# Optimization experiments

Measured on AMD Instinct MI355X. Metric: run time of the kernel, lower is better.

## Reference

```python
import jax, jax.numpy as jnp
import numpy as np
from jax import lax

ALPHA = 1.5
N_ITER = 100


def entmax(z, alpha=ALPHA, n_iter=N_ITER):
    # z: [B, Sq, Sk] scores. Bisection for the entmax threshold tau.
    z = (alpha - 1.0) * z.astype(jnp.float32)
    S = z.shape[-1]
    z_max = jnp.max(z, axis=-1, keepdims=True)          # [B, Sq, 1]
    tau_min = z_max - 1.0
    tau_max = z_max - np.float32(S ** (1.0 - alpha))
    inv = 1.0 / (alpha - 1.0)                            # = 2.0 for alpha=1.5

    def body(carry, _):
        tmin, tmax, _ = carry
        tau = (tmin + tmax) * 0.5
        p = jnp.maximum(z - tau, 0.0) ** inv             # [B, Sq, Sk]
        Z = jnp.sum(p, axis=-1, keepdims=True)           # [B, Sq, 1]
        tmin = jnp.where(Z >= 1.0, tau, tmin)
        tmax = jnp.where(Z < 1.0, tau, tmax)
        return (tmin, tmax, tau), None

    init = (tau_min, tau_max, (tau_min + tau_max) * 0.5)
    (tmin, tmax, tau), _ = lax.scan(jax.checkpoint(body), init, None, length=n_iter)
    # faithful to the TF code: final output uses p, Z from the LAST iteration's tau
    p = jnp.maximum(z - tau, 0.0) ** inv
    Z = jnp.sum(p, axis=-1, keepdims=True)
    return p / Z


def setup_inputs() -> dict:
    key = jax.random.key(0)
    kq, kk, kv = jax.random.split(key, 3)
    B, S, D = 8, 2048, 128
    return {
        "query": jax.random.normal(kq, (B, S, D), dtype=jnp.float32),
        "key": jax.random.normal(kk, (B, S, D), dtype=jnp.float32),
        "value": jax.random.normal(kv, (B, S, D), dtype=jnp.float32),
    }


def reference(query, key, value):
    scores = jnp.einsum("bqd,bkd->bqk", query, key)      # QK^T, no scaling (as in source)
    weights = entmax(scores, alpha=ALPHA, n_iter=N_ITER)
    return jnp.einsum("bqk,bkd->bqd", weights, value)
```

## Files before the change

kernel.cpp:

```cpp
#include <hip/hip_runtime.h>

#define BB 8
#define SS 2048
#define DD 128
#define ROWS 16
#define NW 8
#define CTW 16

typedef short bf16x8 __attribute__((ext_vector_type(8)));
typedef float f32x4 __attribute__((ext_vector_type(4)));

template <int I> struct IC { static constexpr int value = I; };
template <int I, int N, typename F>
__device__ __forceinline__ void sfor(F&& f) {
  if constexpr (I < N) { f(IC<I>{}); sfor<I + 1, N>((F&&)f); }
}

__device__ __forceinline__ short f2bf(float x) {
  return __builtin_bit_cast(short, (__bf16)x);
}

__device__ __forceinline__ void stage_tile(const short* g, short* l) {
#pragma unroll
  for (int s = 0; s < 4; ++s) {
    __builtin_amdgcn_global_load_lds(
        (const __attribute__((address_space(1))) void*)(g + (s << 9)),
        (__attribute__((address_space(3))) void*)(l + (s << 9)), 16, 0, 0);
  }
}

__global__ __launch_bounds__(256)
void ksplit(const float* __restrict__ K, short* __restrict__ Khi) {
  const int lin = blockIdx.x * 256 + threadIdx.x;
  const int r   = lin >> 4;
  const int c8  = lin & 15;
  const float4 v0 = *(const float4*)(K + (size_t)lin * 8);
  const float4 v1 = *(const float4*)(K + (size_t)lin * 8 + 4);
  bf16x8 h;
  h[0] = f2bf(v0.x); h[1] = f2bf(v0.y); h[2] = f2bf(v0.z); h[3] = f2bf(v0.w);
  h[4] = f2bf(v1.x); h[5] = f2bf(v1.y); h[6] = f2bf(v1.z); h[7] = f2bf(v1.w);
  const int bct  = r >> 4;
  const int m16  = r & 15;
  const int s    = c8 >> 2;
  const int quad = c8 & 3;
  const size_t out = ((((size_t)bct * 4 + s) * 64) + quad * 16 + m16) * 8;
  *(bf16x8*)(Khi + out) = h;
}

__global__ __launch_bounds__(512) __attribute__((amdgpu_waves_per_eu(3, 4)))
void attn(const float* __restrict__ Q, const short* __restrict__ Khi,
          const float* __restrict__ K, const float* __restrict__ V,
          float* __restrict__ Out) {
  __shared__ short kring[NW][2][2048];
  __shared__ unsigned short Qs[ROWS][136];
  __shared__ float rbuf[ROWS][64];
  __shared__ int   scol[ROWS][64];
  __shared__ float exM[NW][ROWS];
  __shared__ int   rcnt[ROWS];
  __shared__ int   rovf[ROWS];
  __shared__ float tauB[ROWS], ZB[ROWS];

  const int tid  = threadIdx.x;
  const int lane = tid & 63;
  const int wid  = __builtin_amdgcn_readfirstlane(tid >> 6);
  const int quad = lane >> 4, m16 = lane & 15;
  const int b    = blockIdx.x & 7;
  const int qt   = blockIdx.x >> 3;

  const float* Qb = Q + (size_t)(b * SS + qt * ROWS) * DD;
  const float* Kb = K + (size_t)b * SS * DD;
  const float* Vb = V + (size_t)b * SS * DD;
  float*       Ob = Out + (size_t)(b * SS + qt * ROWS) * DD;
  const short* KHb = Khi + (size_t)b * SS * DD;

  if (tid < ROWS) { rcnt[tid] = 0; rovf[tid] = 0; }

  {
    const int row = tid >> 5, d = (tid & 31) * 4;
    const float4 v = *(const float4*)&Qb[row * DD + d];
    ushort4 h;
    h.x = (unsigned short)f2bf(0.5f * v.x);
    h.y = (unsigned short)f2bf(0.5f * v.y);
    h.z = (unsigned short)f2bf(0.5f * v.z);
    h.w = (unsigned short)f2bf(0.5f * v.w);
    *(ushort4*)&Qs[row][d] = h;
  }
  __syncthreads();

  bf16x8 qh[4];
#pragma unroll
  for (int s = 0; s < 4; ++s)
    qh[s] = *(const bf16x8*)&Qs[m16][s * 32 + quad * 8];

  short* ring0 = &kring[wid][0][0];
  short* ring1 = &kring[wid][1][0];
  const short* gw = KHb + ((size_t)(wid * CTW) << 11) + lane * 8;

  stage_tile(gw + 0 * 2048, ring0);
  stage_tile(gw + 1 * 2048, ring1);

  f32x4 acc[CTW];
  sfor<0, CTW>([&](auto ic) {
    constexpr int i = ic.value;
    if constexpr (i < CTW - 1) asm volatile("s_waitcnt vmcnt(4)" ::: "memory");
    else                       asm volatile("s_waitcnt vmcnt(0)" ::: "memory");
    const short* sbl = ((i & 1) ? ring1 : ring0) + lane * 8;
    f32x4 c = {0.f, 0.f, 0.f, 0.f};
    sfor<0, 4>([&](auto sc) {
      constexpr int s = sc.value;
      const bf16x8 bh = *(const bf16x8*)(sbl + (s << 9));
      c = __builtin_amdgcn_mfma_f32_16x16x32_bf16(qh[s], bh, c, 0, 0, 0);
    });
    acc[i] = c;
    if constexpr (i + 2 < CTW) {
      asm volatile("s_waitcnt lgkmcnt(0)" ::: "memory");
      stage_tile(gw + (i + 2) * 2048, (i & 1) ? ring1 : ring0);
    }
  });

  float mx[4] = {-1e38f, -1e38f, -1e38f, -1e38f};
  sfor<0, CTW>([&](auto ic) {
#pragma unroll
    for (int j = 0; j < 4; ++j) mx[j] = fmaxf(mx[j], acc[ic.value][j]);
  });
#pragma unroll
  for (int j = 0; j < 4; ++j)
#pragma unroll
    for (int s = 1; s <= 8; s <<= 1) mx[j] = fmaxf(mx[j], __shfl_xor(mx[j], s));
  if (m16 == 0) {
#pragma unroll
    for (int j = 0; j < 4; ++j) exM[wid][4 * quad + j] = mx[j];
  }
  __syncthreads();
  float M4[4];
#pragma unroll
  for (int j = 0; j < 4; ++j) {
    float m = -1e38f;
#pragma unroll
    for (int w = 0; w < NW; ++w) m = fmaxf(m, exM[w][4 * quad + j]);
    M4[j] = m;
  }

  sfor<0, CTW>([&](auto ic) {
    constexpr int i = ic.value;
    const int col = wid * 256 + i * 16 + m16;
#pragma unroll
    for (int j = 0; j < 4; ++j) {
      const int row = 4 * quad + j;
      if (acc[i][j] > M4[j] - 1.25f) {
        const int pos = atomicAdd(&rcnt[row], 1);
        if (pos < 64) { scol[row][pos] = col; rbuf[row][pos] = acc[i][j]; }
        else rovf[row] = 1;
      }
    }
  });
  __syncthreads();

  const int rr32 = lane >> 5;
  const int row  = 2 * wid + rr32;
  const int l32  = lane & 31;
  const int nA = rcnt[2 * wid]     < 64 ? rcnt[2 * wid]     : 64;
  const int nB = rcnt[2 * wid + 1] < 64 ? rcnt[2 * wid + 1] : 64;
  const int nr  = rr32 ? nB : nA;
  const int nmx = nA > nB ? nA : nB;

  {
    const float4 q4 = *(const float4*)&Qb[row * DD + l32 * 4];
    for (int i = 0; i < nmx; ++i) {
      const bool act = i < nr;
      const int c = act ? scol[row][i] : scol[row][0];
      const float4 k4 = *(const float4*)&Kb[(size_t)c * DD + l32 * 4];
      float t = q4.x * k4.x + q4.y * k4.y + q4.z * k4.z + q4.w * k4.w;
#pragma unroll
      for (int s = 1; s <= 16; s <<= 1) t += __shfl_xor(t, s);
      if (act && l32 == 0) rbuf[row][i] = 0.5f * t;
    }
  }

  {
    const float z0 = (l32 < nr)      ? rbuf[row][l32]      : -1e38f;
    const float z1 = (l32 + 32 < nr) ? rbuf[row][l32 + 32] : -1e38f;
    float k0 = 0.f, S10 = 0.f, S20 = 0.f, nb0 = -1e38f;
    float k1 = 0.f, S11 = 0.f, S21 = 0.f, nb1 = -1e38f;
    for (int j = 0; j < nr; ++j) {
      const float w = rbuf[row][j];
      const bool ge0 = (w > z0) || (w == z0 && j <= l32);
      k0  += ge0 ? 1.f : 0.f;
      S10 += ge0 ? w : 0.f;
      S20  = ge0 ? fmaf(w, w, S20) : S20;
      nb0  = (!ge0 && w > nb0) ? w : nb0;
      const bool ge1 = (w > z1) || (w == z1 && j <= l32 + 32);
      k1  += ge1 ? 1.f : 0.f;
      S11 += ge1 ? w : 0.f;
      S21  = ge1 ? fmaf(w, w, S21) : S21;
      nb1  = (!ge1 && w > nb1) ? w : nb1;
    }
    const float d0 = fmaxf(fmaf(S10, S10, -k0 * (S20 - 1.f)), 0.f);
    const float d1 = fmaxf(fmaf(S11, S11, -k1 * (S21 - 1.f)), 0.f);
    const float tau0 = (S10 - __builtin_sqrtf(d0)) / fmaxf(k0, 1.f);
    const float tau1 = (S11 - __builtin_sqrtf(d1)) / fmaxf(k1, 1.f);
    const bool v0b = z0 > tau0, v1b = z1 > tau1;
    const bool v0  = v0b && (nb0 <= tau0);
    const bool v1  = v1b && (nb1 <= tau1);
    float tv = fmaxf(v0 ? tau0 : -1e38f, v1 ? tau1 : -1e38f);
    float tb = fmaxf(v0b ? tau0 : -1e38f, v1b ? tau1 : -1e38f);
#pragma unroll
    for (int s = 1; s <= 16; s <<= 1) {
      tv = fmaxf(tv, __shfl_xor(tv, s));
      tb = fmaxf(tb, __shfl_xor(tb, s));
    }
    const float tau = (tv > -1e37f) ? tv : tb;
    const float p0 = fmaxf(z0 - tau, 0.f);
    const float p1 = fmaxf(z1 - tau, 0.f);
    float zp = fmaf(p0, p0, p1 * p1);
#pragma unroll
    for (int s = 1; s <= 16; s <<= 1) zp += __shfl_xor(zp, s);
    if (l32 == 0) { tauB[row] = tau; ZB[row] = zp; }
  }

  if (!rovf[row]) {
    const float tau = tauB[row];
    const float iz  = 1.0f / ZB[row];
    float4 o = {0.f, 0.f, 0.f, 0.f};
    for (int i = 0; i < nr; ++i) {
      const float rv = rbuf[row][i];
      const float tt = fmaxf(rv - tau, 0.f);
      const float pi = tt * tt * iz;
      const int   c  = scol[row][i];
      const float4 v4 = *(const float4*)&Vb[(size_t)c * DD + l32 * 4];
      o.x = fmaf(pi, v4.x, o.x);
      o.y = fmaf(pi, v4.y, o.y);
      o.z = fmaf(pi, v4.z, o.z);
      o.w = fmaf(pi, v4.w, o.w);
    }
    *(float4*)&Ob[row * DD + l32 * 4] = o;
  }

#pragma unroll
  for (int rr = 0; rr < 2; ++rr) {
    const int frow = 2 * wid + rr;
    if (!rovf[frow]) continue;
    float* zr = (float*)&kring[wid][0][0];
    for (int c0 = 0; c0 < 32; ++c0) {
      const int c = c0 * 64 + lane;
      const float* kp = &Kb[(size_t)c * DD];
      float t = 0.f;
      for (int d = 0; d < DD; d += 4) {
        const float4 qv = *(const float4*)&Qb[frow * DD + d];
        const float4 kv = *(const float4*)&kp[d];
        t = fmaf(qv.x, kv.x, t); t = fmaf(qv.y, kv.y, t);
        t = fmaf(qv.z, kv.z, t); t = fmaf(qv.w, kv.w, t);
      }
      zr[c] = 0.5f * t;
    }
    float Mr = -1e38f;
    for (int c0 = 0; c0 < 32; ++c0) Mr = fmaxf(Mr, zr[c0 * 64 + lane]);
#pragma unroll
    for (int s = 1; s <= 32; s <<= 1) Mr = fmaxf(Mr, __shfl_xor(Mr, s));
    float tmn = Mr - 1.0f, tmx = Mr - 0.022097086912079608f;
    float tau = 0.5f * (tmn + tmx), Zr = 0.f;
    for (int it = 0; it < 100; ++it) {
      tau = 0.5f * (tmn + tmx);
      float zp = 0.f;
      for (int c0 = 0; c0 < 32; ++c0) {
        const float tt = fmaxf(zr[c0 * 64 + lane] - tau, 0.f);
        zp = fmaf(tt, tt, zp);
      }
#pragma unroll
      for (int s = 1; s <= 32; s <<= 1) zp += __shfl_xor(zp, s);
      Zr = zp;
      const float nmn = (zp >= 1.f) ? tau : tmn;
      const float nmx2 = (zp >= 1.f) ? tmx : tau;
      const bool ch = (nmn != tmn) || (nmx2 != tmx);
      tmn = nmn; tmx = nmx2;
      if (!__any(ch)) break;
    }
    const float iz = 1.0f / Zr;
    float2 o = {0.f, 0.f};
    for (int c = 0; c < SS; ++c) {
      const float tt = fmaxf(zr[c] - tau, 0.f);
      if (tt > 0.f) {
        const float pi = tt * tt * iz;
        const float2 v2 = *(const float2*)&Vb[(size_t)c * DD + lane * 2];
        o.x = fmaf(pi, v2.x, o.x);
        o.y = fmaf(pi, v2.y, o.y);
      }
    }
    *(float2*)&Ob[frow * DD + lane * 2] = o;
  }
}

extern "C" void kernel_launch(void* const* d_in, const int* in_sizes, int n_in,
                              void* d_out, int out_size, void* d_ws, size_t ws_size,
                              hipStream_t stream) {
  const float* Q = (const float*)d_in[0];
  const float* K = (const float*)d_in[1];
  const float* V = (const float*)d_in[2];
  float* out = (float*)d_out;
  short* Khi = (short*)d_ws;

  hipLaunchKernelGGL(ksplit, dim3(BB * SS * DD / (256 * 8)), dim3(256), 0, stream,
                     K, Khi);
  hipLaunchKernelGGL(attn, dim3(BB * (SS / ROWS)), dim3(512), 0, stream,
                     Q, Khi, K, V, out);
}
```

Measured before the change: 117.0 us.

## Deepen K-tile ring to four stages and restructure candidate rescoring and PV loops

Grows the per-wave LDS ring for the bf16 K tiles from two to four buffers, so four tiles are in flight and the vmcnt waits are adjusted to match. The fp32 rescoring of candidate columns changes from one candidate per iteration with a 32-lane shuffle reduction to one candidate per lane with a full 128-element serial dot product. The PV accumulation loop is unrolled by four with masked tail entries so more V loads are in flight. The larger ring doubles the LDS footprint, which may lower occupancy, and the per-lane dot products read K rows with strided, uncoalesced access.

```diff
diff --git a/kernel.cpp b/kernel.cpp
--- a/kernel.cpp
+++ b/kernel.cpp
@@ -18,6 +18,13 @@
 
 __device__ __forceinline__ short f2bf(float x) {
   return __builtin_bit_cast(short, (__bf16)x);
+}
+
+template <int N> __device__ __forceinline__ void wait_vm() {
+  if constexpr (N >= 12)      asm volatile("s_waitcnt vmcnt(12)" ::: "memory");
+  else if constexpr (N == 8)  asm volatile("s_waitcnt vmcnt(8)" ::: "memory");
+  else if constexpr (N == 4)  asm volatile("s_waitcnt vmcnt(4)" ::: "memory");
+  else                        asm volatile("s_waitcnt vmcnt(0)" ::: "memory");
 }
 
 __device__ __forceinline__ void stage_tile(const short* g, short* l) {
@@ -51,7 +58,7 @@
 void attn(const float* __restrict__ Q, const short* __restrict__ Khi,
           const float* __restrict__ K, const float* __restrict__ V,
           float* __restrict__ Out) {
-  __shared__ short kring[NW][2][2048];
+  __shared__ short kring[NW][4][2048];
   __shared__ unsigned short Qs[ROWS][136];
   __shared__ float rbuf[ROWS][64];
   __shared__ int   scol[ROWS][64];
@@ -92,19 +99,19 @@
   for (int s = 0; s < 4; ++s)
     qh[s] = *(const bf16x8*)&Qs[m16][s * 32 + quad * 8];
 
-  short* ring0 = &kring[wid][0][0];
-  short* ring1 = &kring[wid][1][0];
+  short* ring = &kring[wid][0][0];
   const short* gw = KHb + ((size_t)(wid * CTW) << 11) + lane * 8;
 
-  stage_tile(gw + 0 * 2048, ring0);
-  stage_tile(gw + 1 * 2048, ring1);
+  sfor<0, 4>([&](auto pc) {
+    constexpr int p = pc.value;
+    stage_tile(gw + p * 2048, ring + p * 2048);
+  });
 
   f32x4 acc[CTW];
   sfor<0, CTW>([&](auto ic) {
     constexpr int i = ic.value;
-    if constexpr (i < CTW - 1) asm volatile("s_waitcnt vmcnt(4)" ::: "memory");
-    else                       asm volatile("s_waitcnt vmcnt(0)" ::: "memory");
-    const short* sbl = ((i & 1) ? ring1 : ring0) + lane * 8;
+    wait_vm<(15 - i >= 3 ? 12 : 4 * (15 - i))>();
+    const short* sbl = ring + ((i & 3) << 11) + lane * 8;
     f32x4 c = {0.f, 0.f, 0.f, 0.f};
     sfor<0, 4>([&](auto sc) {
       constexpr int s = sc.value;
@@ -112,9 +119,9 @@
       c = __builtin_amdgcn_mfma_f32_16x16x32_bf16(qh[s], bh, c, 0, 0, 0);
     });
     acc[i] = c;
-    if constexpr (i + 2 < CTW) {
+    if constexpr (i + 4 < CTW) {
       asm volatile("s_waitcnt lgkmcnt(0)" ::: "memory");
-      stage_tile(gw + (i + 2) * 2048, (i & 1) ? ring1 : ring0);
+      stage_tile(gw + (i + 4) * 2048, ring + ((i & 3) << 11));
     }
   });
 
@@ -162,18 +169,36 @@
   const int nA = rcnt[2 * wid]     < 64 ? rcnt[2 * wid]     : 64;
   const int nB = rcnt[2 * wid + 1] < 64 ? rcnt[2 * wid + 1] : 64;
   const int nr  = rr32 ? nB : nA;
-  const int nmx = nA > nB ? nA : nB;
 
   {
-    const float4 q4 = *(const float4*)&Qb[row * DD + l32 * 4];
-    for (int i = 0; i < nmx; ++i) {
-      const bool act = i < nr;
-      const int c = act ? scol[row][i] : scol[row][0];
-      const float4 k4 = *(const float4*)&Kb[(size_t)c * DD + l32 * 4];
-      float t = q4.x * k4.x + q4.y * k4.y + q4.z * k4.z + q4.w * k4.w;
-#pragma unroll
-      for (int s = 1; s <= 16; s <<= 1) t += __shfl_xor(t, s);
-      if (act && l32 == 0) rbuf[row][i] = 0.5f * t;
+    const float4* qp4 = (const float4*)&Qb[row * DD];
+    if (l32 < nr) {
+      const float4* kp4 = (const float4*)&Kb[(size_t)scol[row][l32] * DD];
+      f32x4 t = {0.f, 0.f, 0.f, 0.f};
+#pragma unroll 8
+      for (int d = 0; d < 32; ++d) {
+        const float4 qv = qp4[d];
+        const float4 kv = kp4[d];
+        t[0] = fmaf(qv.x, kv.x, t[0]);
+        t[1] = fmaf(qv.y, kv.y, t[1]);
+        t[2] = fmaf(qv.z, kv.z, t[2]);
+        t[3] = fmaf(qv.w, kv.w, t[3]);
+      }
+      rbuf[row][l32] = 0.5f * ((t[0] + t[1]) + (t[2] + t[3]));
+    }
+    if (nr > 32 && l32 + 32 < nr) {
+      const float4* kp4 = (const float4*)&Kb[(size_t)scol[row][l32 + 32] * DD];
+      f32x4 t = {0.f, 0.f, 0.f, 0.f};
+#pragma unroll 8
+      for (int d = 0; d < 32; ++d) {
+        const float4 qv = qp4[d];
+        const float4 kv = kp4[d];
+        t[0] = fmaf(qv.x, kv.x, t[0]);
+        t[1] = fmaf(qv.y, kv.y, t[1]);
+        t[2] = fmaf(qv.z, kv.z, t[2]);
+        t[3] = fmaf(qv.w, kv.w, t[3]);
+      }
+      rbuf[row][l32 + 32] = 0.5f * ((t[0] + t[1]) + (t[2] + t[3]));
     }
   }
 
@@ -222,16 +247,21 @@
     const float tau = tauB[row];
     const float iz  = 1.0f / ZB[row];
     float4 o = {0.f, 0.f, 0.f, 0.f};
-    for (int i = 0; i < nr; ++i) {
-      const float rv = rbuf[row][i];
-      const float tt = fmaxf(rv - tau, 0.f);
-      const float pi = tt * tt * iz;
-      const int   c  = scol[row][i];
-      const float4 v4 = *(const float4*)&Vb[(size_t)c * DD + l32 * 4];
-      o.x = fmaf(pi, v4.x, o.x);
-      o.y = fmaf(pi, v4.y, o.y);
-      o.z = fmaf(pi, v4.z, o.z);
-      o.w = fmaf(pi, v4.w, o.w);
+    for (int i = 0; i < nr; i += 4) {
+#pragma unroll
+      for (int k = 0; k < 4; ++k) {
+        const bool act = (i + k) < nr;
+        const int  idx = act ? i + k : 0;
+        const float rv = rbuf[row][idx];
+        const float tt = fmaxf(rv - tau, 0.f);
+        const float pi = act ? tt * tt * iz : 0.f;
+        const int   c  = scol[row][idx];
+        const float4 v4 = *(const float4*)&Vb[(size_t)c * DD + l32 * 4];
+        o.x = fmaf(pi, v4.x, o.x);
+        o.y = fmaf(pi, v4.y, o.y);
+        o.z = fmaf(pi, v4.z, o.z);
+        o.w = fmaf(pi, v4.w, o.w);
+      }
     }
     *(float4*)&Ob[row * DD + l32 * 4] = o;
   }
```

Result: slower. 136.8 us (+17.0%).

## Process 32 query rows per block, reusing each staged K tile across two MFMA groups

Applied to the files above, without the earlier changes.

Each block now handles 32 query rows instead of 16. Every staged bf16 K tile feeds two MFMA accumulators, which halves the number of blocks and the total K streaming traffic. To keep register pressure down, the score tiles are kept as packed bf16 pairs instead of f32, and the row max is computed while the MFMAs run. In exchange, the candidate-selection threshold is widened to allow for the bf16 rounding, the per-wave refinement and PV work doubles, and fewer blocks may leave CUs underused.

```diff
diff --git a/kernel.cpp b/kernel.cpp
--- a/kernel.cpp
+++ b/kernel.cpp
@@ -3,7 +3,7 @@
 #define BB 8
 #define SS 2048
 #define DD 128
-#define ROWS 16
+#define ROWS 32
 #define NW 8
 #define CTW 16
 
@@ -18,6 +18,10 @@
 
 __device__ __forceinline__ short f2bf(float x) {
   return __builtin_bit_cast(short, (__bf16)x);
+}
+__device__ __forceinline__ unsigned pk2(float a, float b) {
+  return (unsigned)(unsigned short)f2bf(a) |
+         ((unsigned)(unsigned short)f2bf(b) << 16);
 }
 
 __device__ __forceinline__ void stage_tile(const short* g, short* l) {
@@ -76,21 +80,29 @@
   if (tid < ROWS) { rcnt[tid] = 0; rovf[tid] = 0; }
 
   {
-    const int row = tid >> 5, d = (tid & 31) * 4;
-    const float4 v = *(const float4*)&Qb[row * DD + d];
-    ushort4 h;
-    h.x = (unsigned short)f2bf(0.5f * v.x);
-    h.y = (unsigned short)f2bf(0.5f * v.y);
-    h.z = (unsigned short)f2bf(0.5f * v.z);
-    h.w = (unsigned short)f2bf(0.5f * v.w);
-    *(ushort4*)&Qs[row][d] = h;
+    const int row = tid >> 4, d = (tid & 15) * 8;
+    const float4 v0 = *(const float4*)&Qb[row * DD + d];
+    const float4 v1 = *(const float4*)&Qb[row * DD + d + 4];
+    ushort4 h0, h1;
+    h0.x = (unsigned short)f2bf(0.5f * v0.x);
+    h0.y = (unsigned short)f2bf(0.5f * v0.y);
+    h0.z = (unsigned short)f2bf(0.5f * v0.z);
+    h0.w = (unsigned short)f2bf(0.5f * v0.w);
+    h1.x = (unsigned short)f2bf(0.5f * v1.x);
+    h1.y = (unsigned short)f2bf(0.5f * v1.y);
+    h1.z = (unsigned short)f2bf(0.5f * v1.z);
+    h1.w = (unsigned short)f2bf(0.5f * v1.w);
+    *(ushort4*)&Qs[row][d]     = h0;
+    *(ushort4*)&Qs[row][d + 4] = h1;
   }
   __syncthreads();
 
-  bf16x8 qh[4];
-#pragma unroll
-  for (int s = 0; s < 4; ++s)
-    qh[s] = *(const bf16x8*)&Qs[m16][s * 32 + quad * 8];
+  bf16x8 qh[2][4];
+#pragma unroll
+  for (int g = 0; g < 2; ++g)
+#pragma unroll
+    for (int s = 0; s < 4; ++s)
+      qh[g][s] = *(const bf16x8*)&Qs[g * 16 + m16][s * 32 + quad * 8];
 
   short* ring0 = &kring[wid][0][0];
   short* ring1 = &kring[wid][1][0];
@@ -99,146 +111,173 @@
   stage_tile(gw + 0 * 2048, ring0);
   stage_tile(gw + 1 * 2048, ring1);
 
-  f32x4 acc[CTW];
+  unsigned zpk[2][CTW][2];
+  float mx[2][4] = {{-1e38f, -1e38f, -1e38f, -1e38f},
+                    {-1e38f, -1e38f, -1e38f, -1e38f}};
+
   sfor<0, CTW>([&](auto ic) {
     constexpr int i = ic.value;
     if constexpr (i < CTW - 1) asm volatile("s_waitcnt vmcnt(4)" ::: "memory");
     else                       asm volatile("s_waitcnt vmcnt(0)" ::: "memory");
     const short* sbl = ((i & 1) ? ring1 : ring0) + lane * 8;
-    f32x4 c = {0.f, 0.f, 0.f, 0.f};
+    f32x4 cA = {0.f, 0.f, 0.f, 0.f};
+    f32x4 cB = {0.f, 0.f, 0.f, 0.f};
     sfor<0, 4>([&](auto sc) {
       constexpr int s = sc.value;
       const bf16x8 bh = *(const bf16x8*)(sbl + (s << 9));
-      c = __builtin_amdgcn_mfma_f32_16x16x32_bf16(qh[s], bh, c, 0, 0, 0);
+      cA = __builtin_amdgcn_mfma_f32_16x16x32_bf16(qh[0][s], bh, cA, 0, 0, 0);
+      cB = __builtin_amdgcn_mfma_f32_16x16x32_bf16(qh[1][s], bh, cB, 0, 0, 0);
     });
-    acc[i] = c;
+#pragma unroll
+    for (int j = 0; j < 4; ++j) {
+      mx[0][j] = fmaxf(mx[0][j], cA[j]);
+      mx[1][j] = fmaxf(mx[1][j], cB[j]);
+    }
+    zpk[0][i][0] = pk2(cA[0], cA[1]);
+    zpk[0][i][1] = pk2(cA[2], cA[3]);
+    zpk[1][i][0] = pk2(cB[0], cB[1]);
+    zpk[1][i][1] = pk2(cB[2], cB[3]);
     if constexpr (i + 2 < CTW) {
       asm volatile("s_waitcnt lgkmcnt(0)" ::: "memory");
       stage_tile(gw + (i + 2) * 2048, (i & 1) ? ring1 : ring0);
     }
   });
 
-  float mx[4] = {-1e38f, -1e38f, -1e38f, -1e38f};
-  sfor<0, CTW>([&](auto ic) {
-#pragma unroll
-    for (int j = 0; j < 4; ++j) mx[j] = fmaxf(mx[j], acc[ic.value][j]);
-  });
-#pragma unroll
-  for (int j = 0; j < 4; ++j)
-#pragma unroll
-    for (int s = 1; s <= 8; s <<= 1) mx[j] = fmaxf(mx[j], __shfl_xor(mx[j], s));
+#pragma unroll
+  for (int g = 0; g < 2; ++g)
+#pragma unroll
+    for (int j = 0; j < 4; ++j)
+#pragma unroll
+      for (int s = 1; s <= 8; s <<= 1)
+        mx[g][j] = fmaxf(mx[g][j], __shfl_xor(mx[g][j], s));
   if (m16 == 0) {
 #pragma unroll
-    for (int j = 0; j < 4; ++j) exM[wid][4 * quad + j] = mx[j];
+    for (int g = 0; g < 2; ++g)
+#pragma unroll
+      for (int j = 0; j < 4; ++j) exM[wid][g * 16 + 4 * quad + j] = mx[g][j];
   }
   __syncthreads();
-  float M4[4];
-#pragma unroll
-  for (int j = 0; j < 4; ++j) {
-    float m = -1e38f;
-#pragma unroll
-    for (int w = 0; w < NW; ++w) m = fmaxf(m, exM[w][4 * quad + j]);
-    M4[j] = m;
-  }
-
-  sfor<0, CTW>([&](auto ic) {
-    constexpr int i = ic.value;
-    const int col = wid * 256 + i * 16 + m16;
+  float M4[2][4];
+#pragma unroll
+  for (int g = 0; g < 2; ++g)
 #pragma unroll
     for (int j = 0; j < 4; ++j) {
-      const int row = 4 * quad + j;
-      if (acc[i][j] > M4[j] - 1.25f) {
-        const int pos = atomicAdd(&rcnt[row], 1);
-        if (pos < 64) { scol[row][pos] = col; rbuf[row][pos] = acc[i][j]; }
-        else rovf[row] = 1;
+      float m = -1e38f;
+#pragma unroll
+      for (int w = 0; w < NW; ++w) m = fmaxf(m, exM[w][g * 16 + 4 * quad + j]);
+      M4[g][j] = m;
+    }
+
+  sfor<0, CTW>([&](auto cc) {
+    constexpr int ct = cc.value;
+    const int col = wid * 256 + ct * 16 + m16;
+#pragma unroll
+    for (int g = 0; g < 2; ++g) {
+      float v[4];
+      v[0] = __uint_as_float(zpk[g][ct][0] << 16);
+      v[1] = __uint_as_float(zpk[g][ct][0] & 0xffff0000u);
+      v[2] = __uint_as_float(zpk[g][ct][1] << 16);
+      v[3] = __uint_as_float(zpk[g][ct][1] & 0xffff0000u);
+#pragma unroll
+      for (int j = 0; j < 4; ++j) {
+        const int row = g * 16 + 4 * quad + j;
+        if (v[j] > M4[g][j] - 1.35f) {
+          const int pos = atomicAdd(&rcnt[row], 1);
+          if (pos < 64) { scol[row][pos] = col; rbuf[row][pos] = v[j]; }
+          else rovf[row] = 1;
+        }
       }
     }
   });
   __syncthreads();
 
   const int rr32 = lane >> 5;
-  const int row  = 2 * wid + rr32;
   const int l32  = lane & 31;
-  const int nA = rcnt[2 * wid]     < 64 ? rcnt[2 * wid]     : 64;
-  const int nB = rcnt[2 * wid + 1] < 64 ? rcnt[2 * wid + 1] : 64;
-  const int nr  = rr32 ? nB : nA;
-  const int nmx = nA > nB ? nA : nB;
-
-  {
-    const float4 q4 = *(const float4*)&Qb[row * DD + l32 * 4];
-    for (int i = 0; i < nmx; ++i) {
-      const bool act = i < nr;
-      const int c = act ? scol[row][i] : scol[row][0];
-      const float4 k4 = *(const float4*)&Kb[(size_t)c * DD + l32 * 4];
-      float t = q4.x * k4.x + q4.y * k4.y + q4.z * k4.z + q4.w * k4.w;
-#pragma unroll
-      for (int s = 1; s <= 16; s <<= 1) t += __shfl_xor(t, s);
-      if (act && l32 == 0) rbuf[row][i] = 0.5f * t;
-    }
-  }
-
-  {
-    const float z0 = (l32 < nr)      ? rbuf[row][l32]      : -1e38f;
-    const float z1 = (l32 + 32 < nr) ? rbuf[row][l32 + 32] : -1e38f;
-    float k0 = 0.f, S10 = 0.f, S20 = 0.f, nb0 = -1e38f;
-    float k1 = 0.f, S11 = 0.f, S21 = 0.f, nb1 = -1e38f;
-    for (int j = 0; j < nr; ++j) {
-      const float w = rbuf[row][j];
-      const bool ge0 = (w > z0) || (w == z0 && j <= l32);
-      k0  += ge0 ? 1.f : 0.f;
-      S10 += ge0 ? w : 0.f;
-      S20  = ge0 ? fmaf(w, w, S20) : S20;
-      nb0  = (!ge0 && w > nb0) ? w : nb0;
-      const bool ge1 = (w > z1) || (w == z1 && j <= l32 + 32);
-      k1  += ge1 ? 1.f : 0.f;
-      S11 += ge1 ? w : 0.f;
-      S21  = ge1 ? fmaf(w, w, S21) : S21;
-      nb1  = (!ge1 && w > nb1) ? w : nb1;
-    }
-    const float d0 = fmaxf(fmaf(S10, S10, -k0 * (S20 - 1.f)), 0.f);
-    const float d1 = fmaxf(fmaf(S11, S11, -k1 * (S21 - 1.f)), 0.f);
-    const float tau0 = (S10 - __builtin_sqrtf(d0)) / fmaxf(k0, 1.f);
-    const float tau1 = (S11 - __builtin_sqrtf(d1)) / fmaxf(k1, 1.f);
-    const bool v0b = z0 > tau0, v1b = z1 > tau1;
-    const bool v0  = v0b && (nb0 <= tau0);
-    const bool v1  = v1b && (nb1 <= tau1);
-    float tv = fmaxf(v0 ? tau0 : -1e38f, v1 ? tau1 : -1e38f);
-    float tb = fmaxf(v0b ? tau0 : -1e38f, v1b ? tau1 : -1e38f);
-#pragma unroll
-    for (int s = 1; s <= 16; s <<= 1) {
-      tv = fmaxf(tv, __shfl_xor(tv, s));
-      tb = fmaxf(tb, __shfl_xor(tb, s));
-    }
-    const float tau = (tv > -1e37f) ? tv : tb;
-    const float p0 = fmaxf(z0 - tau, 0.f);
-    const float p1 = fmaxf(z1 - tau, 0.f);
-    float zp = fmaf(p0, p0, p1 * p1);
-#pragma unroll
-    for (int s = 1; s <= 16; s <<= 1) zp += __shfl_xor(zp, s);
-    if (l32 == 0) { tauB[row] = tau; ZB[row] = zp; }
-  }
-
-  if (!rovf[row]) {
-    const float tau = tauB[row];
-    const float iz  = 1.0f / ZB[row];
-    float4 o = {0.f, 0.f, 0.f, 0.f};
-    for (int i = 0; i < nr; ++i) {
-      const float rv = rbuf[row][i];
-      const float tt = fmaxf(rv - tau, 0.f);
-      const float pi = tt * tt * iz;
-      const int   c  = scol[row][i];
-      const float4 v4 = *(const float4*)&Vb[(size_t)c * DD + l32 * 4];
-      o.x = fmaf(pi, v4.x, o.x);
-      o.y = fmaf(pi, v4.y, o.y);
-      o.z = fmaf(pi, v4.z, o.z);
-      o.w = fmaf(pi, v4.w, o.w);
-    }
-    *(float4*)&Ob[row * DD + l32 * 4] = o;
-  }
-
-#pragma unroll
-  for (int rr = 0; rr < 2; ++rr) {
-    const int frow = 2 * wid + rr;
+
+#pragma unroll
+  for (int p = 0; p < 2; ++p) {
+    const int row = 4 * wid + 2 * p + rr32;
+    const int nA = rcnt[4 * wid + 2 * p]     < 64 ? rcnt[4 * wid + 2 * p]     : 64;
+    const int nB = rcnt[4 * wid + 2 * p + 1] < 64 ? rcnt[4 * wid + 2 * p + 1] : 64;
+    const int nr  = rr32 ? nB : nA;
+    const int nmx = nA > nB ? nA : nB;
+
+    {
+      const float4 q4 = *(const float4*)&Qb[row * DD + l32 * 4];
+      for (int i = 0; i < nmx; ++i) {
+        const bool act = i < nr;
+        const int c = act ? scol[row][i] : scol[row][0];
+        const float4 k4 = *(const float4*)&Kb[(size_t)c * DD + l32 * 4];
+        float t = q4.x * k4.x + q4.y * k4.y + q4.z * k4.z + q4.w * k4.w;
+#pragma unroll
+        for (int s = 1; s <= 16; s <<= 1) t += __shfl_xor(t, s);
+        if (act && l32 == 0) rbuf[row][i] = 0.5f * t;
+      }
+    }
+
+    {
+      const float z0 = (l32 < nr)      ? rbuf[row][l32]      : -1e38f;
+      const float z1 = (l32 + 32 < nr) ? rbuf[row][l32 + 32] : -1e38f;
+      float k0 = 0.f, S10 = 0.f, S20 = 0.f, nb0 = -1e38f;
+      float k1 = 0.f, S11 = 0.f, S21 = 0.f, nb1 = -1e38f;
+      for (int j = 0; j < nr; ++j) {
+        const float w = rbuf[row][j];
+        const bool ge0 = (w > z0) || (w == z0 && j <= l32);
+        k0  += ge0 ? 1.f : 0.f;
+        S10 += ge0 ? w : 0.f;
+        S20  = ge0 ? fmaf(w, w, S20) : S20;
+        nb0  = (!ge0 && w > nb0) ? w : nb0;
+        const bool ge1 = (w > z1) || (w == z1 && j <= l32 + 32);
+        k1  += ge1 ? 1.f : 0.f;
+        S11 += ge1 ? w : 0.f;
+        S21  = ge1 ? fmaf(w, w, S21) : S21;
+        nb1  = (!ge1 && w > nb1) ? w : nb1;
+      }
+      const float d0 = fmaxf(fmaf(S10, S10, -k0 * (S20 - 1.f)), 0.f);
+      const float d1 = fmaxf(fmaf(S11, S11, -k1 * (S21 - 1.f)), 0.f);
+      const float tau0 = (S10 - __builtin_sqrtf(d0)) / fmaxf(k0, 1.f);
+      const float tau1 = (S11 - __builtin_sqrtf(d1)) / fmaxf(k1, 1.f);
+      const bool v0b = z0 > tau0, v1b = z1 > tau1;
+      const bool v0  = v0b && (nb0 <= tau0);
+      const bool v1  = v1b && (nb1 <= tau1);
+      float tv = fmaxf(v0 ? tau0 : -1e38f, v1 ? tau1 : -1e38f);
+      float tb = fmaxf(v0b ? tau0 : -1e38f, v1b ? tau1 : -1e38f);
+#pragma unroll
+      for (int s = 1; s <= 16; s <<= 1) {
+        tv = fmaxf(tv, __shfl_xor(tv, s));
+        tb = fmaxf(tb, __shfl_xor(tb, s));
+      }
+      const float tau = (tv > -1e37f) ? tv : tb;
+      const float p0 = fmaxf(z0 - tau, 0.f);
+      const float p1 = fmaxf(z1 - tau, 0.f);
+      float zp = fmaf(p0, p0, p1 * p1);
+#pragma unroll
+      for (int s = 1; s <= 16; s <<= 1) zp += __shfl_xor(zp, s);
+      if (l32 == 0) { tauB[row] = tau; ZB[row] = zp; }
+    }
+
+    if (!rovf[row]) {
+      const float tau = tauB[row];
+      const float iz  = 1.0f / ZB[row];
+      float4 o = {0.f, 0.f, 0.f, 0.f};
+      for (int i = 0; i < nr; ++i) {
+        const float rv = rbuf[row][i];
+        const float tt = fmaxf(rv - tau, 0.f);
+        const float pi = tt * tt * iz;
+        const int   c  = scol[row][i];
+        const float4 v4 = *(const float4*)&Vb[(size_t)c * DD + l32 * 4];
+        o.x = fmaf(pi, v4.x, o.x);
+        o.y = fmaf(pi, v4.y, o.y);
+        o.z = fmaf(pi, v4.z, o.z);
+        o.w = fmaf(pi, v4.w, o.w);
+      }
+      *(float4*)&Ob[row * DD + l32 * 4] = o;
+    }
+  }
+
+#pragma unroll
+  for (int rr = 0; rr < 4; ++rr) {
+    const int frow = 4 * wid + rr;
     if (!rovf[frow]) continue;
     float* zr = (float*)&kring[wid][0][0];
     for (int c0 = 0; c0 < 32; ++c0) {
```

Result: slower. 121.1 us (+3.6%).
